# Kernel tuning notes

Hardware: AMD Instinct MI355X
Metric: run time of the kernel (lower is better)

The kernel has to match this reference:

```python
import jax, jax.numpy as jnp
import numpy as np

MARGIN = 0.4
SCALE = 80.0
NEG_FILL = -1e30  # used instead of -inf for masked logsumexp (keeps grads NaN-free)

N, D, NUM_CLASSES = 8192, 128, 512


def setup_inputs() -> dict:
    key = jax.random.key(0)
    k1, k2 = jax.random.split(key)
    embeds = jax.random.normal(k1, (N, D), dtype=jnp.float32)
    labels = jax.random.randint(k2, (N,), 0, NUM_CLASSES, dtype=jnp.int64)
    return {"embeds": embeds, "labels": labels}


def _masked_lse(terms, mask):
    # stable logsumexp over axis=1 restricted to mask
    t = jnp.where(mask, terms, NEG_FILL)
    m = jnp.max(t, axis=1, keepdims=True)
    return jnp.squeeze(m, 1) + jnp.log(jnp.sum(jnp.exp(t - m), axis=1))


def reference(embeds, labels):
    # L2-normalize embeddings (F.normalize, p=2, dim=1, eps=1e-12)
    norm = jnp.maximum(jnp.linalg.norm(embeds, axis=1, keepdims=True), 1e-12)
    e = embeds / norm
    sim = e @ e.T  # [N, N]

    same = labels[:, None] == labels[None, :]
    eye = jnp.eye(labels.shape[0], dtype=bool)
    pos_mask = same & ~eye          # positives for each anchor (row)
    neg_mask = ~same                # negatives for each anchor

    # alphas are computed under no_grad in the original
    ap_alpha = jax.lax.stop_gradient(jax.nn.relu(1.0 + MARGIN - sim))
    an_alpha = jax.lax.stop_gradient(jax.nn.relu(sim + MARGIN))

    ap_term = -SCALE * ap_alpha * (sim - 1.0 + MARGIN)
    an_term = SCALE * an_alpha * (sim - MARGIN)

    np_cnt = jnp.sum(pos_mask, axis=1)  # positives per anchor
    nn_cnt = jnp.sum(neg_mask, axis=1)  # negatives per anchor
    valid = (np_cnt > 0) & (nn_cnt > 0)

    # All-triplets logsumexp factorizes: LSE over (p,n) pairs of ap_term[p]
    # equals LSE over p + log(num_neg); symmetric for an_term.
    lse_p = _masked_lse(ap_term, pos_mask)
    lse_n = _masked_lse(an_term, neg_mask)
    log_np = jnp.where(valid, jnp.log(np_cnt.astype(sim.dtype)), 0.0)
    log_nn = jnp.where(valid, jnp.log(nn_cnt.astype(sim.dtype)), 0.0)

    loss_i = jax.nn.softplus(lse_p + log_nn + lse_n + log_np)
    loss = jnp.sum(jnp.where(valid, loss_i, 0.0)) / jnp.maximum(
        jnp.sum(valid).astype(sim.dtype), 1.0)
    return loss
```

## Files before the change

kernel.cpp:

```cpp
#include <hip/hip_runtime.h>
#include <hip/hip_bf16.h>

#define NN_ 8192
#define DD_ 128
#define NSPLIT 32
#define JSPLIT (NN_ / NSPLIT)
#define NORMB 512
#define NCLS 512
#define CAP 48
#define LVP 132

typedef short bf16x8 __attribute__((ext_vector_type(8)));
typedef float f32x4 __attribute__((ext_vector_type(4)));
union U4 { uint4 u; bf16x8 h; };

#if __has_builtin(__builtin_amdgcn_exp2f)
#define EXP2(x) __builtin_amdgcn_exp2f(x)
#else
#define EXP2(x) __expf((x) * 0.69314718056f)
#endif

#define C1 115.415603f
#define LN2 0.69314718056f

__device__ __forceinline__ unsigned short f2bf(float f) {
    unsigned int u = __float_as_uint(f);
    unsigned int r = (u + 0x7FFFu + ((u >> 16) & 1u)) >> 16;
    return (unsigned short)r;
}


__global__ __launch_bounds__(256) void k_norm_pos(const float* __restrict__ x,
                                                  const int* __restrict__ labels,
                                                  unsigned short* __restrict__ ebf,
                                                  float* __restrict__ posout,
                                                  unsigned int* __restrict__ zinit) {
    __shared__ int lmem[CAP];
    __shared__ int lcnt;
    __shared__ float lvec[CAP * LVP];
    __shared__ float pairS[CAP * CAP];

    const int t = threadIdx.x;
    const int bid = blockIdx.x;

    if (bid < NORMB) {
        int r16 = t >> 4;
        int g = t & 15;
        int row = bid * 16 + r16;
        const float4* xr = (const float4*)(x + (size_t)row * DD_);
        float4 v0 = xr[g * 2];
        float4 v1 = xr[g * 2 + 1];
        float ss = v0.x * v0.x + v0.y * v0.y + v0.z * v0.z + v0.w * v0.w +
                   v1.x * v1.x + v1.y * v1.y + v1.z * v1.z + v1.w * v1.w;
#pragma unroll
        for (int m = 1; m < 16; m <<= 1) ss += __shfl_xor(ss, m);
        float inv = 1.0f / fmaxf(sqrtf(ss), 1e-12f);
        float vs[8] = {v0.x, v0.y, v0.z, v0.w, v1.x, v1.y, v1.z, v1.w};
        unsigned int p[4];
#pragma unroll
        for (int k = 0; k < 4; k++) {
            unsigned short lo = f2bf(vs[2 * k] * inv);
            unsigned short hi = f2bf(vs[2 * k + 1] * inv);
            p[k] = (unsigned int)lo | ((unsigned int)hi << 16);
        }
        uint4 out = {p[0], p[1], p[2], p[3]};
        ((uint4*)ebf)[bid * 256 + g * 16 + r16] = out;
        if (bid == 0 && t < 3) zinit[t] = 0u;
        return;
    }

    const int c = bid - NORMB;
    if (t == 0) lcnt = 0;
    __syncthreads();
    for (int idx = t; idx < NN_; idx += 256) {
        if (labels[idx] == c) {
            int p = atomicAdd(&lcnt, 1);
            if (p < CAP) lmem[p] = idx;
        }
    }
    __syncthreads();
    int cnt = min(lcnt, CAP);

    for (int base = 0; base < cnt; base += 16) {
        int lr = base + (t >> 4);
        int g = t & 15;
        bool valid = lr < cnt;
        int row = lmem[valid ? lr : 0];
        const float4* xr = (const float4*)(x + (size_t)row * DD_);
        float4 v0 = xr[g * 2];
        float4 v1 = xr[g * 2 + 1];
        float ss = v0.x * v0.x + v0.y * v0.y + v0.z * v0.z + v0.w * v0.w +
                   v1.x * v1.x + v1.y * v1.y + v1.z * v1.z + v1.w * v1.w;
#pragma unroll
        for (int m = 1; m < 16; m <<= 1) ss += __shfl_xor(ss, m);
        float inv = 1.0f / fmaxf(sqrtf(ss), 1e-12f);
        if (valid) {
            float vs[8] = {v0.x, v0.y, v0.z, v0.w, v1.x, v1.y, v1.z, v1.w};
#pragma unroll
            for (int k = 0; k < 8; k++) {
                unsigned short h = f2bf(vs[k] * inv);
                lvec[lr * LVP + g * 8 + k] = __uint_as_float(((unsigned int)h) << 16);
            }
        }
    }
    __syncthreads();

    int npair = cnt * cnt;
    for (int p = t; p < npair; p += 256) {
        int a2 = p / cnt, b2 = p - a2 * cnt;
        float s = 0.0f;
#pragma unroll 16
        for (int d = 0; d < 128; d++)
            s = fmaf(lvec[a2 * LVP + d], lvec[b2 * LVP + d], s);
        pairS[p] = s;
    }
    __syncthreads();

    if (t < cnt) {
        float mx = -1e30f;
        for (int b2 = 0; b2 < cnt; b2++) {
            if (b2 == t) continue;
            float s = pairS[t * cnt + b2];
            float al = fmaxf(1.4f - s, 0.0f) * (-C1);
            mx = fmaxf(mx, al * (s - 0.6f));
        }
        float sp = 0.0f, ssum = 0.0f;
        for (int b2 = 0; b2 < cnt; b2++) {
            if (b2 == t) continue;
            float s = pairS[t * cnt + b2];
            float al = fmaxf(1.4f - s, 0.0f) * (-C1);
            sp += EXP2(al * (s - 0.6f) - mx);
            ssum += EXP2(fmaf(s * C1, s, -C1));
        }
        float4 o = {mx, sp, ssum, (float)cnt};
        ((float4*)posout)[lmem[t]] = o;
    }
}

__global__ __launch_bounds__(512, 4) void k_main(const unsigned short* __restrict__ ebf,
                                                 float* __restrict__ states) {
    const int lane = threadIdx.x & 63;
    const int wave = threadIdx.x >> 6;
    const int quad = lane >> 4;
    const int lcol = lane & 15;
    const int jsplit = blockIdx.x & 31;
    const int by = blockIdx.x >> 5;
    const int rowbase = by * 256 + wave * 32;
    const int j0 = jsplit * JSPLIT;

    const uint4* fb = (const uint4*)ebf;

    U4 afr[2][4];
#pragma unroll
    for (int h = 0; h < 2; h++)
#pragma unroll
        for (int kc = 0; kc < 4; kc++)
            afr[h][kc].u = fb[((rowbase >> 4) + h) * 256 + kc * 64 + lane];

    float S_an[8] = {0.f, 0.f, 0.f, 0.f, 0.f, 0.f, 0.f, 0.f};

    U4 b0[4], b1[4];
#pragma unroll
    for (int kc = 0; kc < 4; kc++) b0[kc].u = fb[(j0 >> 4) * 256 + kc * 64 + lane];
#pragma unroll
    for (int kc = 0; kc < 4; kc++) b1[kc].u = fb[((j0 + 16) >> 4) * 256 + kc * 64 + lane];

    const int NIT = JSPLIT / 32;
    for (int it = 0; it < NIT; ++it) {
        const int jt = j0 + it * 32;
        const int jp = (it + 1 < NIT) ? jt + 32 : j0;

        {
            f32x4 a0 = {0.f, 0.f, 0.f, 0.f}, a1 = {0.f, 0.f, 0.f, 0.f};
#pragma unroll
            for (int kc = 0; kc < 4; kc++)
                a0 = __builtin_amdgcn_mfma_f32_16x16x32_bf16(afr[0][kc].h, b0[kc].h, a0, 0, 0, 0);
#pragma unroll
            for (int kc = 0; kc < 4; kc++)
                a1 = __builtin_amdgcn_mfma_f32_16x16x32_bf16(afr[1][kc].h, b0[kc].h, a1, 0, 0, 0);
            bool d0 = (jt == rowbase), d1 = (jt == rowbase + 16);
#pragma unroll
            for (int r = 0; r < 4; r++) {
                float s0 = a0[r], s1 = a1[r];
                float e0 = EXP2(fmaf(s0 * C1, s0, -C1));
                float e1 = EXP2(fmaf(s1 * C1, s1, -C1));
                if (d0 && lcol == quad * 4 + r) e0 = 0.0f;
                if (d1 && lcol == quad * 4 + r) e1 = 0.0f;
                S_an[r] += e0;
                S_an[4 + r] += e1;
            }
        }
#pragma unroll
        for (int kc = 0; kc < 4; kc++) b0[kc].u = fb[(jp >> 4) * 256 + kc * 64 + lane];

        {
            f32x4 a0 = {0.f, 0.f, 0.f, 0.f}, a1 = {0.f, 0.f, 0.f, 0.f};
#pragma unroll
            for (int kc = 0; kc < 4; kc++)
                a0 = __builtin_amdgcn_mfma_f32_16x16x32_bf16(afr[0][kc].h, b1[kc].h, a0, 0, 0, 0);
#pragma unroll
            for (int kc = 0; kc < 4; kc++)
                a1 = __builtin_amdgcn_mfma_f32_16x16x32_bf16(afr[1][kc].h, b1[kc].h, a1, 0, 0, 0);
            bool d0 = (jt + 16 == rowbase), d1 = (jt + 16 == rowbase + 16);
#pragma unroll
            for (int r = 0; r < 4; r++) {
                float s0 = a0[r], s1 = a1[r];
                float e0 = EXP2(fmaf(s0 * C1, s0, -C1));
                float e1 = EXP2(fmaf(s1 * C1, s1, -C1));
                if (d0 && lcol == quad * 4 + r) e0 = 0.0f;
                if (d1 && lcol == quad * 4 + r) e1 = 0.0f;
                S_an[r] += e0;
                S_an[4 + r] += e1;
            }
        }
#pragma unroll
        for (int kc = 0; kc < 4; kc++) b1[kc].u = fb[((jp + 16) >> 4) * 256 + kc * 64 + lane];
    }

#pragma unroll
    for (int hr = 0; hr < 8; hr++)
#pragma unroll
        for (int m = 1; m < 16; m <<= 1) S_an[hr] += __shfl_xor(S_an[hr], m);

    if (lcol == 0) {
#pragma unroll
        for (int h = 0; h < 2; h++)
#pragma unroll
            for (int r = 0; r < 4; r++) {
                int i = rowbase + h * 16 + quad * 4 + r;
                states[(size_t)i * NSPLIT + jsplit] = S_an[h * 4 + r];
            }
    }
}

__global__ __launch_bounds__(256) void k_fin(const float* __restrict__ states,
                                             const float* __restrict__ posout,
                                             float* __restrict__ accum,
                                             unsigned int* __restrict__ ticket,
                                             float* __restrict__ out) {
    int i = blockIdx.x * 256 + threadIdx.x;
    float4 po = ((const float4*)posout)[i];
    float S = 0.0f;
#pragma unroll
    for (int k = 0; k < NSPLIT; k++) S += states[(size_t)i * NSPLIT + k];
    S -= po.z;
    int cnt = (int)po.w;
    int np = cnt - 1, nn = NN_ - cnt;
    float loss = 0.0f, v = 0.0f;
    if (np > 0 && nn > 0 && po.y > 0.0f && S > 0.0f) {
        float lse_p = LN2 * po.x + __logf(po.y);
        float lse_n = 67.2f + __logf(S);
        float z = lse_p + lse_n + __logf((float)np) + __logf((float)nn);
        loss = fmaxf(z, 0.0f) + log1pf(__expf(-fabsf(z)));
        v = 1.0f;
    }
#pragma unroll
    for (int m = 1; m < 64; m <<= 1) {
        loss += __shfl_xor(loss, m);
        v += __shfl_xor(v, m);
    }
    if ((threadIdx.x & 63) == 0) {
        atomicAdd(&accum[0], loss);
        atomicAdd(&accum[1], v);
    }
    __syncthreads();
    if (threadIdx.x == 0) {
        __threadfence();
        unsigned int old = atomicAdd(ticket, 1u);
        if (old == gridDim.x - 1) {
            float L = atomicAdd(&accum[0], 0.0f);
            float V = atomicAdd(&accum[1], 0.0f);
            out[0] = L / fmaxf(V, 1.0f);
        }
    }
}

extern "C" void kernel_launch(void* const* d_in, const int* in_sizes, int n_in,
                              void* d_out, int out_size, void* d_ws, size_t ws_size,
                              hipStream_t stream) {
    const float* embeds = (const float*)d_in[0];
    const int* labels = (const int*)d_in[1];
    float* out = (float*)d_out;

    char* ws = (char*)d_ws;
    unsigned short* ebf = (unsigned short*)ws;
    float* states = (float*)(ws + 2097152);
    float* posout = (float*)(ws + 2097152 + 1048576);
    float* accum = (float*)(ws + 2097152 + 1048576 + 131072);
    unsigned int* ticket = (unsigned int*)(ws + 2097152 + 1048576 + 131072 + 8);

    k_norm_pos<<<NORMB + NCLS, 256, 0, stream>>>(embeds, labels, ebf, posout,
                                                 (unsigned int*)accum);
    k_main<<<NN_ / 256 * NSPLIT, 512, 0, stream>>>(ebf, states);
    k_fin<<<NN_ / 256, 256, 0, stream>>>(states, posout, accum, ticket, out);
}
```

Baseline: 104.8 us.

## Fuse final reduction into main kernel via per-row-group completion counters

Removes the separate finalize kernel launch. The last block to finish each 256-row group, detected with an atomic counter, reduces the partial sums for that group and adds to the global accumulator. A ticket counter then picks the final block, which writes the loss. The partial-state layout also changes to split-major, so the finalizing reads are coalesced. This saves one launch and its gap, at the cost of extra fences and atomics in every block and a serial tail on the last blocks.

```diff
diff --git a/kernel.cpp b/kernel.cpp
--- a/kernel.cpp
+++ b/kernel.cpp
@@ -9,6 +9,7 @@
 #define NCLS 512
 #define CAP 48
 #define LVP 132
+#define NGRP 32
 
 typedef short bf16x8 __attribute__((ext_vector_type(8)));
 typedef float f32x4 __attribute__((ext_vector_type(4)));
@@ -30,11 +31,12 @@
 }
 
 
+
 __global__ __launch_bounds__(256) void k_norm_pos(const float* __restrict__ x,
                                                   const int* __restrict__ labels,
                                                   unsigned short* __restrict__ ebf,
                                                   float* __restrict__ posout,
-                                                  unsigned int* __restrict__ zinit) {
+                                                  unsigned int* __restrict__ ctrl) {
     __shared__ int lmem[CAP];
     __shared__ int lcnt;
     __shared__ float lvec[CAP * LVP];
@@ -65,7 +67,7 @@
         }
         uint4 out = {p[0], p[1], p[2], p[3]};
         ((uint4*)ebf)[bid * 256 + g * 16 + r16] = out;
-        if (bid == 0 && t < 3) zinit[t] = 0u;
+        if (bid == 0 && t < 35) ctrl[t] = 0u;
         return;
     }
 
@@ -137,10 +139,19 @@
     }
 }
 
-__global__ __launch_bounds__(512, 4) void k_main(const unsigned short* __restrict__ ebf,
-                                                 float* __restrict__ states) {
-    const int lane = threadIdx.x & 63;
-    const int wave = threadIdx.x >> 6;
+__global__ __launch_bounds__(512, 4) void k_main_fin(const unsigned short* __restrict__ ebf,
+                                                     float* __restrict__ states,
+                                                     const float* __restrict__ posout,
+                                                     unsigned int* __restrict__ ctrl,
+                                                     float* __restrict__ out) {
+    __shared__ int isLast;
+    float* accum = (float*)ctrl;
+    unsigned int* ticket = ctrl + 2;
+    unsigned int* grpcnt = ctrl + 3;
+
+    const int t = threadIdx.x;
+    const int lane = t & 63;
+    const int wave = t >> 6;
     const int quad = lane >> 4;
     const int lcol = lane & 15;
     const int jsplit = blockIdx.x & 31;
@@ -228,46 +239,51 @@
 #pragma unroll
             for (int r = 0; r < 4; r++) {
                 int i = rowbase + h * 16 + quad * 4 + r;
-                states[(size_t)i * NSPLIT + jsplit] = S_an[h * 4 + r];
+                states[(size_t)jsplit * NN_ + i] = S_an[h * 4 + r];
             }
     }
-}
-
-__global__ __launch_bounds__(256) void k_fin(const float* __restrict__ states,
-                                             const float* __restrict__ posout,
-                                             float* __restrict__ accum,
-                                             unsigned int* __restrict__ ticket,
-                                             float* __restrict__ out) {
-    int i = blockIdx.x * 256 + threadIdx.x;
-    float4 po = ((const float4*)posout)[i];
-    float S = 0.0f;
-#pragma unroll
-    for (int k = 0; k < NSPLIT; k++) S += states[(size_t)i * NSPLIT + k];
-    S -= po.z;
-    int cnt = (int)po.w;
-    int np = cnt - 1, nn = NN_ - cnt;
+
+    __threadfence();
+    __syncthreads();
+    if (t == 0) {
+        unsigned int old = atomicAdd(&grpcnt[by], 1u);
+        isLast = (old == NSPLIT - 1) ? 1 : 0;
+    }
+    __syncthreads();
+    if (!isLast) return;
+
     float loss = 0.0f, v = 0.0f;
-    if (np > 0 && nn > 0 && po.y > 0.0f && S > 0.0f) {
-        float lse_p = LN2 * po.x + __logf(po.y);
-        float lse_n = 67.2f + __logf(S);
-        float z = lse_p + lse_n + __logf((float)np) + __logf((float)nn);
-        loss = fmaxf(z, 0.0f) + log1pf(__expf(-fabsf(z)));
-        v = 1.0f;
+    if (t < 256) {
+        int row = by * 256 + t;
+        float S = 0.0f;
+#pragma unroll
+        for (int k = 0; k < NSPLIT; k++) S += states[(size_t)k * NN_ + row];
+        float4 po = ((const float4*)posout)[row];
+        S -= po.z;
+        int cnt = (int)po.w;
+        int np = cnt - 1, nn = NN_ - cnt;
+        if (np > 0 && nn > 0 && po.y > 0.0f && S > 0.0f) {
+            float lse_p = LN2 * po.x + __logf(po.y);
+            float lse_n = 67.2f + __logf(S);
+            float z = lse_p + lse_n + __logf((float)np) + __logf((float)nn);
+            loss = fmaxf(z, 0.0f) + log1pf(__expf(-fabsf(z)));
+            v = 1.0f;
+        }
     }
 #pragma unroll
     for (int m = 1; m < 64; m <<= 1) {
         loss += __shfl_xor(loss, m);
         v += __shfl_xor(v, m);
     }
-    if ((threadIdx.x & 63) == 0) {
+    if (lane == 0 && wave < 4) {
         atomicAdd(&accum[0], loss);
         atomicAdd(&accum[1], v);
     }
     __syncthreads();
-    if (threadIdx.x == 0) {
+    if (t == 0) {
         __threadfence();
         unsigned int old = atomicAdd(ticket, 1u);
-        if (old == gridDim.x - 1) {
+        if (old == NGRP - 1) {
             float L = atomicAdd(&accum[0], 0.0f);
             float V = atomicAdd(&accum[1], 0.0f);
             out[0] = L / fmaxf(V, 1.0f);
@@ -286,11 +302,8 @@
     unsigned short* ebf = (unsigned short*)ws;
     float* states = (float*)(ws + 2097152);
     float* posout = (float*)(ws + 2097152 + 1048576);
-    float* accum = (float*)(ws + 2097152 + 1048576 + 131072);
-    unsigned int* ticket = (unsigned int*)(ws + 2097152 + 1048576 + 131072 + 8);
-
-    k_norm_pos<<<NORMB + NCLS, 256, 0, stream>>>(embeds, labels, ebf, posout,
-                                                 (unsigned int*)accum);
-    k_main<<<NN_ / 256 * NSPLIT, 512, 0, stream>>>(ebf, states);
-    k_fin<<<NN_ / 256, 256, 0, stream>>>(states, posout, accum, ticket, out);
+    unsigned int* ctrl = (unsigned int*)(ws + 2097152 + 1048576 + 131072);
+
+    k_norm_pos<<<NORMB + NCLS, 256, 0, stream>>>(embeds, labels, ebf, posout, ctrl);
+    k_main_fin<<<NGRP * NSPLIT, 512, 0, stream>>>(ebf, states, posout, ctrl, out);
 }
```

Result: slower. 244.9 us (+133.7%).
